# Optimization experiments

Hardware: AMD Instinct MI355X
Metric: run time of the kernel (lower is better)

## Reference

```python
import jax, jax.numpy as jnp
import numpy as np

THRESH = 0.5  # original code thresholds raw span logit channel 0 at 0.5


def setup_inputs() -> dict:
    key = jax.random.key(0)
    ks = jax.random.split(key, 9)
    B, S, H, P = 4, 256, 768, 54  # P = num_spo_patterns + 1
    scale = 0.02
    return {
        "sequence_output": jax.random.normal(ks[0], (B, S, H), jnp.float32),
        "W1s": jax.random.normal(ks[1], (H, H), jnp.float32) * scale,
        "b1s": jnp.zeros((H,), jnp.float32),
        "W2s": jax.random.normal(ks[2], (2, H), jnp.float32) * scale,
        "b2s": jnp.zeros((2,), jnp.float32),
        "Wp1": jax.random.normal(ks[3], (H, 2 * H), jnp.float32) * scale,
        "bp1": jnp.zeros((H,), jnp.float32),
        "Wp2": jax.random.normal(ks[4], (P, H), jnp.float32) * scale,
        "bp2": jnp.zeros((P,), jnp.float32),
    }


def reference(sequence_output, W1s, b1s, W2s, b2s, Wp1, bp1, Wp2, bp2):
    x = sequence_output                                # [B,S,H]
    B, S, H = x.shape
    # span classifier: Linear -> ReLU -> Linear
    h = jax.nn.relu(jnp.einsum('bsh,kh->bsk', x, W1s) + b1s)
    span_logits = jnp.einsum('bsh,kh->bsk', h, W2s) + b2s   # [B,S,2]
    cand = span_logits[..., 0] > THRESH                      # [B,S] candidates
    # spo pattern classifier on concat pairs: Linear(2H,H) splits into two H->H maps
    Wa, Wb = Wp1[:, :H], Wp1[:, H:]                          # subject / object halves
    ha = jnp.einsum('bsh,kh->bsk', x, Wa)                    # [B,S,H]
    hb = jnp.einsum('bsh,kh->bsk', x, Wb)                    # [B,S,H]
    pair_hidden = jax.nn.relu(ha[:, :, None, :] + hb[:, None, :, :] + bp1)  # [B,S,S,H]
    pair_logits = jnp.einsum('bijh,ph->bijp', pair_hidden, Wp2) + bp2       # [B,S,S,P]
    # valid pairs: both are candidates and subj != obj (diagonal excluded)
    not_diag = ~jnp.eye(S, dtype=bool)
    valid = cand[:, :, None] & cand[:, None, :] & not_diag   # [B,S,S]
    # dense masked equivalent of the per-pair Python loop (invalid pairs zeroed,
    # matching the zeros fallback for empty candidate sets)
    spo_pattern_logits = jnp.where(valid[..., None], pair_logits, 0.0)
    return spo_pattern_logits
```

## Files before the change

### kernel.cpp

```cpp
#include <hip/hip_runtime.h>
#include <hip/hip_bf16.h>


#define M_ROWS 1024
#define HDIM 768
#define PDIM 54
#define MAXC 256
#define KCHUNK 16
#define NKC (HDIM / KCHUNK)
#define KSPLIT 8
#define KSEG (HDIM / KSPLIT)

#define PAIRGRID 1024
#define HABGRID  2048

#define CANDCNT_OFF  0
#define PAIRCNT_OFF  4
#define CANDIDX_OFF  8192
#define CANDSLOT_OFF 12288
#define PAIR_OFF     16384
#define HPART_OFF    1064960

__global__ __launch_bounds__(256) void gemm_k_kernel(
    const float* __restrict__ x, const float* __restrict__ W1,
    float* __restrict__ hpart, int* __restrict__ counters)
{
    __shared__ float As[16][132];
    __shared__ float Bs[16][132];

    if (blockIdx.x == 0 && blockIdx.y == 0 && blockIdx.z == 0 && threadIdx.x < 2)
        counters[threadIdx.x] = 0;

    const int m0 = blockIdx.x * 128;
    const int n0 = blockIdx.y * 128;
    const int kb = blockIdx.z * KSEG;
    const int t  = threadIdx.x;
    const int tm = t & 15;
    const int tn = t >> 4;
    const int r  = t >> 2;
    const int c4 = (t & 3) * 4;

    float acc[8][8] = {};

    for (int k0 = kb; k0 < kb + KSEG; k0 += 16) {
        #pragma unroll
        for (int rr = 0; rr < 128; rr += 64) {
            float4 av = *(const float4*)(x  + (size_t)(m0 + rr + r) * HDIM + k0 + c4);
            float4 bv = *(const float4*)(W1 + (size_t)(n0 + rr + r) * HDIM + k0 + c4);
            As[c4+0][rr+r] = av.x; As[c4+1][rr+r] = av.y;
            As[c4+2][rr+r] = av.z; As[c4+3][rr+r] = av.w;
            Bs[c4+0][rr+r] = bv.x; Bs[c4+1][rr+r] = bv.y;
            Bs[c4+2][rr+r] = bv.z; Bs[c4+3][rr+r] = bv.w;
        }
        __syncthreads();
        #pragma unroll
        for (int kk = 0; kk < 16; ++kk) {
            float a[8], b[8];
            #pragma unroll
            for (int i = 0; i < 4; ++i) {
                a[i]     = As[kk][tm * 4 + i];
                a[i + 4] = As[kk][64 + tm * 4 + i];
                b[i]     = Bs[kk][tn * 4 + i];
                b[i + 4] = Bs[kk][64 + tn * 4 + i];
            }
            #pragma unroll
            for (int i = 0; i < 8; ++i)
                #pragma unroll
                for (int j = 0; j < 8; ++j)
                    acc[i][j] += a[i] * b[j];
        }
        __syncthreads();
    }

    float* dst = hpart + (size_t)blockIdx.z * (M_ROWS * HDIM);
    #pragma unroll
    for (int ii = 0; ii < 8; ++ii) {
        int row = m0 + (ii >> 2) * 64 + tm * 4 + (ii & 3);
        #pragma unroll
        for (int h = 0; h < 2; ++h) {
            float4 v = make_float4(acc[ii][h*4+0], acc[ii][h*4+1],
                                   acc[ii][h*4+2], acc[ii][h*4+3]);
            *(float4*)(dst + (size_t)row * HDIM + n0 + h * 64 + tn * 4) = v;
        }
    }
}

__global__ __launch_bounds__(256) void span_cand_kernel(
    const float* __restrict__ hpart, const float* __restrict__ b1,
    const float* __restrict__ w2row, const float* __restrict__ b2,
    int* __restrict__ candCount, int* __restrict__ candIdx,
    int* __restrict__ candSlot)
{
    const int m = blockIdx.x;
    const int t = threadIdx.x;
    float p = 0.f;
    for (int n = t; n < HDIM; n += 256) {
        float v = 0.f;
        #pragma unroll
        for (int z = 0; z < KSPLIT; ++z)
            v += hpart[(size_t)z * (M_ROWS * HDIM) + (size_t)m * HDIM + n];
        v += b1[n];
        v = v > 0.f ? v : 0.f;
        p += v * w2row[n];
    }
    __shared__ float wred[4];
    #pragma unroll
    for (int off = 32; off > 0; off >>= 1) p += __shfl_down(p, off, 64);
    if ((t & 63) == 0) wred[t >> 6] = p;
    __syncthreads();
    if (t == 0) {
        float s = wred[0] + wred[1] + wred[2] + wred[3] + b2[0];
        if (s > 0.5f) {
            int sl = atomicAdd(candCount, 1);
            if (sl < MAXC) { candIdx[sl] = m; candSlot[m] = sl; }
            else candSlot[m] = -1;
        } else {
            candSlot[m] = -1;
        }
    }
}

__global__ __launch_bounds__(256) void hab_pairs_kernel(
    const float* __restrict__ x, const float* __restrict__ Wp1,
    const int* __restrict__ candCount, const int* __restrict__ candIdx,
    float* __restrict__ ha, float* __restrict__ hb,
    const int* __restrict__ candSlot,
    int* __restrict__ pairCount, int* __restrict__ pairList,
    float* __restrict__ out)
{
    if (blockIdx.x < PAIRGRID) {
        const int pb = blockIdx.x;
        float4* dst = (float4*)(out + (size_t)pb * 256 * PDIM);
        const float4 z4 = make_float4(0.f, 0.f, 0.f, 0.f);
        for (int f = threadIdx.x; f < 256 * PDIM / 4; f += 256)
            dst[f] = z4;
        int idx = pb * 256 + threadIdx.x;
        int b = idx >> 16;
        int i = (idx >> 8) & 255;
        int j = idx & 255;
        if (i != j && candSlot[b * 256 + i] >= 0 && candSlot[b * 256 + j] >= 0) {
            int p = atomicAdd(pairCount, 1);
            pairList[p] = idx;
        }
        return;
    }

    __shared__ float xs[HDIM];
    __shared__ float red[2][KCHUNK][17];
    int nc = *candCount; if (nc > MAXC) nc = MAXC;
    const int nitems = nc * NKC;
    const int kk  = threadIdx.x >> 4;
    const int hb0 = (threadIdx.x & 15) * 4;

    for (int item = blockIdx.x - PAIRGRID; item < nitems; item += HABGRID) {
        int slot = item / NKC;
        int kc   = item % NKC;
        int row  = candIdx[slot];

        for (int h = threadIdx.x; h < HDIM; h += 256)
            xs[h] = x[(size_t)row * HDIM + h];
        __syncthreads();

        int k = kc * KCHUNK + kk;
        const float* wr = Wp1 + (size_t)k * (2 * HDIM);
        float sa = 0.f, sb = 0.f;
        #pragma unroll
        for (int h = hb0; h < HDIM; h += 64) {
            float4 xv = *(const float4*)(xs + h);
            float4 wa = *(const float4*)(wr + h);
            float4 wb = *(const float4*)(wr + HDIM + h);
            sa += xv.x * wa.x + xv.y * wa.y + xv.z * wa.z + xv.w * wa.w;
            sb += xv.x * wb.x + xv.y * wb.y + xv.z * wb.z + xv.w * wb.w;
        }
        red[0][kk][threadIdx.x & 15] = sa;
        red[1][kk][threadIdx.x & 15] = sb;
        __syncthreads();

        if (threadIdx.x < 32) {
            int which = threadIdx.x >> 4;
            int kk2   = threadIdx.x & 15;
            float s = 0.f;
            #pragma unroll
            for (int g = 0; g < 16; ++g) s += red[which][kk2][g];
            float* dstp = which == 0 ? ha : hb;
            dstp[(size_t)slot * HDIM + kc * KCHUNK + kk2] = s;
        }
        __syncthreads();
    }
}

__global__ __launch_bounds__(256) void pair_kernel(
    const float* __restrict__ ha, const float* __restrict__ hb,
    const float* __restrict__ bp1, const float* __restrict__ Wp2,
    const float* __restrict__ bp2, const int* __restrict__ candSlot,
    const int* __restrict__ pairCount, const int* __restrict__ pairList,
    float* __restrict__ out)
{
    __shared__ float v[HDIM];
    __shared__ float red[4][PDIM + 2];
    const int np = *pairCount;
    const int t = threadIdx.x;
    for (int p = blockIdx.x; p < np; p += gridDim.x) {
        int idx = pairList[p];
        int b = idx >> 16;
        int i = (idx >> 8) & 255;
        int j = idx & 255;
        int si = candSlot[b * 256 + i];
        int sj = candSlot[b * 256 + j];
        if (t < 192) {
            float4 a4 = *(const float4*)(ha + (size_t)si * HDIM + t * 4);
            float4 b4 = *(const float4*)(hb + (size_t)sj * HDIM + t * 4);
            float4 c4 = *(const float4*)(bp1 + t * 4);
            float4 r;
            r.x = a4.x + b4.x + c4.x; r.x = r.x > 0.f ? r.x : 0.f;
            r.y = a4.y + b4.y + c4.y; r.y = r.y > 0.f ? r.y : 0.f;
            r.z = a4.z + b4.z + c4.z; r.z = r.z > 0.f ? r.z : 0.f;
            r.w = a4.w + b4.w + c4.w; r.w = r.w > 0.f ? r.w : 0.f;
            *(float4*)(v + t * 4) = r;
        }
        __syncthreads();
        if (t < 216) {
            int pp  = t % PDIM;
            int seg = t / PDIM;
            const float* w = Wp2 + (size_t)pp * HDIM + seg * 192;
            const float* vv = v + seg * 192;
            float s = 0.f;
            for (int h = 0; h < 192; h += 4) {
                float4 a = *(const float4*)(vv + h);
                float4 b2_ = *(const float4*)(w + h);
                s += a.x * b2_.x + a.y * b2_.y + a.z * b2_.z + a.w * b2_.w;
            }
            red[seg][pp] = s;
        }
        __syncthreads();
        if (t < PDIM)
            out[(size_t)idx * PDIM + t] = red[0][t] + red[1][t] + red[2][t] + red[3][t] + bp2[t];
        __syncthreads();
    }
}

extern "C" void kernel_launch(void* const* d_in, const int* in_sizes, int n_in,
                              void* d_out, int out_size, void* d_ws, size_t ws_size,
                              hipStream_t stream) {
    const float* x   = (const float*)d_in[0];
    const float* W1s = (const float*)d_in[1];
    const float* b1s = (const float*)d_in[2];
    const float* W2s = (const float*)d_in[3];
    const float* b2s = (const float*)d_in[4];
    const float* Wp1 = (const float*)d_in[5];
    const float* bp1 = (const float*)d_in[6];
    const float* Wp2 = (const float*)d_in[7];
    const float* bp2 = (const float*)d_in[8];

    char* ws = (char*)d_ws;
    int*   counters = (int*)(ws + CANDCNT_OFF);
    int*   candCnt  = counters;
    int*   pairCnt  = counters + 1;
    int*   candIdx  = (int*)(ws + CANDIDX_OFF);
    int*   candSlot = (int*)(ws + CANDSLOT_OFF);
    int*   pairList = (int*)(ws + PAIR_OFF);
    float* hpart    = (float*)(ws + HPART_OFF);
    float* ha       = hpart + (size_t)KSPLIT * M_ROWS * HDIM;
    float* hb       = ha + (size_t)MAXC * HDIM;
    float* out = (float*)d_out;

    dim3 g(M_ROWS / 128, HDIM / 128, KSPLIT);
    gemm_k_kernel<<<g, 256, 0, stream>>>(x, W1s, hpart, counters);

    span_cand_kernel<<<M_ROWS, 256, 0, stream>>>(hpart, b1s, W2s, b2s,
                                                 candCnt, candIdx, candSlot);

    hab_pairs_kernel<<<PAIRGRID + HABGRID, 256, 0, stream>>>(
        x, Wp1, candCnt, candIdx, ha, hb, candSlot, pairCnt, pairList, out);

    pair_kernel<<<512, 256, 0, stream>>>(ha, hb, bp1, Wp2, bp2,
                                         candSlot, pairCnt, pairList, out);
}
```

Baseline: 140.9 us.

## Use split-bf16 MFMA for span GEMM and fuse ReLU/W2 reduction into epilogue

Replaces the fp32 split-K SIMT GEMM for the span classifier with a bf16 MFMA kernel. It emulates fp32 precision with three hi/lo products per tile and loads operands straight from global memory into registers. The bias, ReLU and W2 dot product now run in the GEMM epilogue, so it writes only a small per-N-block partial sum instead of eight full hidden partials. A tiny kernel sums those partials and selects candidates. This removes the large hpart write/read traffic and the separate reduction pass, at the cost of a three-term bf16 approximation near the threshold and no shared-memory reuse of the operands.

```diff
diff --git a/kernel.cpp b/kernel.cpp
--- a/kernel.cpp
+++ b/kernel.cpp
@@ -8,115 +8,162 @@
 #define MAXC 256
 #define KCHUNK 16
 #define NKC (HDIM / KCHUNK)
-#define KSPLIT 8
-#define KSEG (HDIM / KSPLIT)
+#define NB_N 12
 
 #define PAIRGRID 1024
 #define HABGRID  2048
 
 #define CANDCNT_OFF  0
-#define PAIRCNT_OFF  4
 #define CANDIDX_OFF  8192
 #define CANDSLOT_OFF 12288
 #define PAIR_OFF     16384
-#define HPART_OFF    1064960
-
-__global__ __launch_bounds__(256) void gemm_k_kernel(
+#define SPAN_OFF     1064960
+
+typedef __attribute__((ext_vector_type(8))) short short8;
+typedef __attribute__((ext_vector_type(4))) float f32x4;
+
+static __device__ __forceinline__ unsigned short f2bf(float f) {
+    unsigned u = __float_as_uint(f);
+    u += 0x7fffu + ((u >> 16) & 1u);
+    return (unsigned short)(u >> 16);
+}
+static __device__ __forceinline__ float bf2f(unsigned short h) {
+    return __uint_as_float(((unsigned)h) << 16);
+}
+static __device__ __forceinline__ void cvt8(float4 p, float4 q,
+                                            short8& hi, short8& lo) {
+    float f[8] = {p.x, p.y, p.z, p.w, q.x, q.y, q.z, q.w};
+    #pragma unroll
+    for (int j = 0; j < 8; ++j) {
+        unsigned short h = f2bf(f[j]);
+        hi[j] = (short)h;
+        lo[j] = (short)f2bf(f[j] - bf2f(h));
+    }
+}
+
+__global__ __launch_bounds__(256) void mfma_span_kernel(
     const float* __restrict__ x, const float* __restrict__ W1,
-    float* __restrict__ hpart, int* __restrict__ counters)
+    const float* __restrict__ b1, const float* __restrict__ w2row,
+    float* __restrict__ spanPart, int* __restrict__ counters)
 {
-    __shared__ float As[16][132];
-    __shared__ float Bs[16][132];
-
-    if (blockIdx.x == 0 && blockIdx.y == 0 && blockIdx.z == 0 && threadIdx.x < 2)
+    if (blockIdx.x == 0 && blockIdx.y == 0 && threadIdx.x < 2)
         counters[threadIdx.x] = 0;
 
-    const int m0 = blockIdx.x * 128;
-    const int n0 = blockIdx.y * 128;
-    const int kb = blockIdx.z * KSEG;
-    const int t  = threadIdx.x;
-    const int tm = t & 15;
-    const int tn = t >> 4;
-    const int r  = t >> 2;
-    const int c4 = (t & 3) * 4;
-
-    float acc[8][8] = {};
-
-    for (int k0 = kb; k0 < kb + KSEG; k0 += 16) {
+    const int t    = threadIdx.x;
+    const int lane = t & 63;
+    const int w    = t >> 6;
+    const int wm   = w >> 1, wn = w & 1;
+    const int l15  = lane & 15;
+    const int lk   = (lane >> 4) * 8;
+    const int m0   = blockIdx.x * 64;
+    const int n0   = blockIdx.y * 64;
+
+    const float* aBase = x  + (size_t)(m0 + wm * 32 + l15) * HDIM + lk;
+    const float* bBase = W1 + (size_t)(n0 + wn * 32 + l15) * HDIM + lk;
+
+    f32x4 acc00 = {0.f, 0.f, 0.f, 0.f};
+    f32x4 acc01 = {0.f, 0.f, 0.f, 0.f};
+    f32x4 acc10 = {0.f, 0.f, 0.f, 0.f};
+    f32x4 acc11 = {0.f, 0.f, 0.f, 0.f};
+
+    float4 ra0p_x, ra0q_x, ra1p_x, ra1q_x, rb0p_x, rb0q_x, rb1p_x, rb1q_x;
+    float4 ra0p_y, ra0q_y, ra1p_y, ra1q_y, rb0p_y, rb0q_y, rb1p_y, rb1q_y;
+
+#define LOADK(sfx, kk) { \
+    ra0p##sfx = *(const float4*)(aBase + (kk));                 \
+    ra0q##sfx = *(const float4*)(aBase + (kk) + 4);             \
+    ra1p##sfx = *(const float4*)(aBase + 16 * HDIM + (kk));     \
+    ra1q##sfx = *(const float4*)(aBase + 16 * HDIM + (kk) + 4); \
+    rb0p##sfx = *(const float4*)(bBase + (kk));                 \
+    rb0q##sfx = *(const float4*)(bBase + (kk) + 4);             \
+    rb1p##sfx = *(const float4*)(bBase + 16 * HDIM + (kk));     \
+    rb1q##sfx = *(const float4*)(bBase + 16 * HDIM + (kk) + 4); \
+}
+
+#define COMPUTE(sfx) { \
+    short8 ah0, al0, ah1, al1, bh0, bl0, bh1, bl1;  \
+    cvt8(ra0p##sfx, ra0q##sfx, ah0, al0);           \
+    cvt8(ra1p##sfx, ra1q##sfx, ah1, al1);           \
+    cvt8(rb0p##sfx, rb0q##sfx, bh0, bl0);           \
+    cvt8(rb1p##sfx, rb1q##sfx, bh1, bl1);           \
+    acc00 = __builtin_amdgcn_mfma_f32_16x16x32_bf16(ah0, bh0, acc00, 0, 0, 0); \
+    acc00 = __builtin_amdgcn_mfma_f32_16x16x32_bf16(ah0, bl0, acc00, 0, 0, 0); \
+    acc00 = __builtin_amdgcn_mfma_f32_16x16x32_bf16(al0, bh0, acc00, 0, 0, 0); \
+    acc01 = __builtin_amdgcn_mfma_f32_16x16x32_bf16(ah0, bh1, acc01, 0, 0, 0); \
+    acc01 = __builtin_amdgcn_mfma_f32_16x16x32_bf16(ah0, bl1, acc01, 0, 0, 0); \
+    acc01 = __builtin_amdgcn_mfma_f32_16x16x32_bf16(al0, bh1, acc01, 0, 0, 0); \
+    acc10 = __builtin_amdgcn_mfma_f32_16x16x32_bf16(ah1, bh0, acc10, 0, 0, 0); \
+    acc10 = __builtin_amdgcn_mfma_f32_16x16x32_bf16(ah1, bl0, acc10, 0, 0, 0); \
+    acc10 = __builtin_amdgcn_mfma_f32_16x16x32_bf16(al1, bh0, acc10, 0, 0, 0); \
+    acc11 = __builtin_amdgcn_mfma_f32_16x16x32_bf16(ah1, bh1, acc11, 0, 0, 0); \
+    acc11 = __builtin_amdgcn_mfma_f32_16x16x32_bf16(ah1, bl1, acc11, 0, 0, 0); \
+    acc11 = __builtin_amdgcn_mfma_f32_16x16x32_bf16(al1, bh1, acc11, 0, 0, 0); \
+}
+
+    LOADK(_x, 0);
+    for (int k = 0; k < HDIM; k += 64) {
+        LOADK(_y, k + 32);
+        COMPUTE(_x);
+        if (k + 64 < HDIM) { LOADK(_x, k + 64); }
+        COMPUTE(_y);
+    }
+#undef LOADK
+#undef COMPUTE
+
+    float sp0[4], sp1[4];
+    #pragma unroll
+    for (int r = 0; r < 4; ++r) { sp0[r] = 0.f; sp1[r] = 0.f; }
+
+#define SPANACC(ACC, SP, J) { \
+    _Pragma("unroll") \
+    for (int r = 0; r < 4; ++r) { \
+        int n = n0 + wn * 32 + (J) * 16 + l15; \
+        float v = ACC[r] + b1[n]; \
+        v = v > 0.f ? v : 0.f; \
+        SP[r] += v * w2row[n]; \
+    } \
+}
+    SPANACC(acc00, sp0, 0)
+    SPANACC(acc01, sp0, 1)
+    SPANACC(acc10, sp1, 0)
+    SPANACC(acc11, sp1, 1)
+#undef SPANACC
+
+    __shared__ float red[64][2];
+    #pragma unroll
+    for (int r = 0; r < 4; ++r) {
+        float v0 = sp0[r], v1 = sp1[r];
         #pragma unroll
-        for (int rr = 0; rr < 128; rr += 64) {
-            float4 av = *(const float4*)(x  + (size_t)(m0 + rr + r) * HDIM + k0 + c4);
-            float4 bv = *(const float4*)(W1 + (size_t)(n0 + rr + r) * HDIM + k0 + c4);
-            As[c4+0][rr+r] = av.x; As[c4+1][rr+r] = av.y;
-            As[c4+2][rr+r] = av.z; As[c4+3][rr+r] = av.w;
-            Bs[c4+0][rr+r] = bv.x; Bs[c4+1][rr+r] = bv.y;
-            Bs[c4+2][rr+r] = bv.z; Bs[c4+3][rr+r] = bv.w;
-        }
-        __syncthreads();
-        #pragma unroll
-        for (int kk = 0; kk < 16; ++kk) {
-            float a[8], b[8];
-            #pragma unroll
-            for (int i = 0; i < 4; ++i) {
-                a[i]     = As[kk][tm * 4 + i];
-                a[i + 4] = As[kk][64 + tm * 4 + i];
-                b[i]     = Bs[kk][tn * 4 + i];
-                b[i + 4] = Bs[kk][64 + tn * 4 + i];
-            }
-            #pragma unroll
-            for (int i = 0; i < 8; ++i)
-                #pragma unroll
-                for (int j = 0; j < 8; ++j)
-                    acc[i][j] += a[i] * b[j];
-        }
-        __syncthreads();
-    }
-
-    float* dst = hpart + (size_t)blockIdx.z * (M_ROWS * HDIM);
-    #pragma unroll
-    for (int ii = 0; ii < 8; ++ii) {
-        int row = m0 + (ii >> 2) * 64 + tm * 4 + (ii & 3);
-        #pragma unroll
-        for (int h = 0; h < 2; ++h) {
-            float4 v = make_float4(acc[ii][h*4+0], acc[ii][h*4+1],
-                                   acc[ii][h*4+2], acc[ii][h*4+3]);
-            *(float4*)(dst + (size_t)row * HDIM + n0 + h * 64 + tn * 4) = v;
-        }
-    }
-}
-
-__global__ __launch_bounds__(256) void span_cand_kernel(
-    const float* __restrict__ hpart, const float* __restrict__ b1,
-    const float* __restrict__ w2row, const float* __restrict__ b2,
+        for (int msk = 1; msk < 16; msk <<= 1) {
+            v0 += __shfl_xor(v0, msk, 64);
+            v1 += __shfl_xor(v1, msk, 64);
+        }
+        if (l15 == 0) {
+            int rr = (lane >> 4) * 4 + r;
+            red[wm * 32 + rr][wn]      = v0;
+            red[wm * 32 + 16 + rr][wn] = v1;
+        }
+    }
+    __syncthreads();
+    if (t < 64)
+        spanPart[(size_t)blockIdx.y * M_ROWS + m0 + t] = red[t][0] + red[t][1];
+}
+
+__global__ __launch_bounds__(256) void cand_kernel(
+    const float* __restrict__ spanPart, const float* __restrict__ b2,
     int* __restrict__ candCount, int* __restrict__ candIdx,
     int* __restrict__ candSlot)
 {
-    const int m = blockIdx.x;
-    const int t = threadIdx.x;
-    float p = 0.f;
-    for (int n = t; n < HDIM; n += 256) {
-        float v = 0.f;
-        #pragma unroll
-        for (int z = 0; z < KSPLIT; ++z)
-            v += hpart[(size_t)z * (M_ROWS * HDIM) + (size_t)m * HDIM + n];
-        v += b1[n];
-        v = v > 0.f ? v : 0.f;
-        p += v * w2row[n];
-    }
-    __shared__ float wred[4];
+    int m = blockIdx.x * 256 + threadIdx.x;
+    float s = b2[0];
     #pragma unroll
-    for (int off = 32; off > 0; off >>= 1) p += __shfl_down(p, off, 64);
-    if ((t & 63) == 0) wred[t >> 6] = p;
-    __syncthreads();
-    if (t == 0) {
-        float s = wred[0] + wred[1] + wred[2] + wred[3] + b2[0];
-        if (s > 0.5f) {
-            int sl = atomicAdd(candCount, 1);
-            if (sl < MAXC) { candIdx[sl] = m; candSlot[m] = sl; }
-            else candSlot[m] = -1;
-        } else {
-            candSlot[m] = -1;
-        }
+    for (int nb = 0; nb < NB_N; ++nb) s += spanPart[(size_t)nb * M_ROWS + m];
+    if (s > 0.5f) {
+        int sl = atomicAdd(candCount, 1);
+        if (sl < MAXC) { candIdx[sl] = m; candSlot[m] = sl; }
+        else candSlot[m] = -1;
+    } else {
+        candSlot[m] = -1;
     }
 }
 
@@ -259,16 +306,15 @@
     int*   candIdx  = (int*)(ws + CANDIDX_OFF);
     int*   candSlot = (int*)(ws + CANDSLOT_OFF);
     int*   pairList = (int*)(ws + PAIR_OFF);
-    float* hpart    = (float*)(ws + HPART_OFF);
-    float* ha       = hpart + (size_t)KSPLIT * M_ROWS * HDIM;
+    float* spanPart = (float*)(ws + SPAN_OFF);
+    float* ha       = spanPart + (size_t)NB_N * M_ROWS;
     float* hb       = ha + (size_t)MAXC * HDIM;
     float* out = (float*)d_out;
 
-    dim3 g(M_ROWS / 128, HDIM / 128, KSPLIT);
-    gemm_k_kernel<<<g, 256, 0, stream>>>(x, W1s, hpart, counters);
-
-    span_cand_kernel<<<M_ROWS, 256, 0, stream>>>(hpart, b1s, W2s, b2s,
-                                                 candCnt, candIdx, candSlot);
+    mfma_span_kernel<<<dim3(M_ROWS / 64, NB_N), 256, 0, stream>>>(
+        x, W1s, b1s, W2s, spanPart, counters);
+
+    cand_kernel<<<4, 256, 0, stream>>>(spanPart, b2s, candCnt, candIdx, candSlot);
 
     hab_pairs_kernel<<<PAIRGRID + HABGRID, 256, 0, stream>>>(
         x, Wp1, candCnt, candIdx, ha, hb, candSlot, pairCnt, pairList, out);
```

New measurement: 134.9 us, median of 2. 1.04x faster.
